# Kernel tuning notes

Measured on AMD Instinct MI355X. Metric: run time of the kernel, lower is better.

## Reference

```python
import jax, jax.numpy as jnp
import numpy as np

S = 8192      # total packed tokens
H = 1152      # hidden size
NH = 16       # heads
HD = 72       # head dim
NSEG = 8      # number of packed (equal-length) sequences
L = S // NSEG # tokens per sequence
SCALE = HD ** -0.5


def setup_inputs() -> dict:
    key = jax.random.key(0)
    ks = jax.random.split(key, 4)
    hidden_states = jax.random.normal(ks[0], (1, S, H), jnp.float32)
    # Real rotary cos/sin per token position within each sequence.
    inv_freq = 1.0 / (10000.0 ** (np.arange(0, HD, 2, dtype=np.float64) / HD))
    freqs = np.outer(np.arange(L, dtype=np.float64), inv_freq)  # [L, HD/2]
    emb = np.concatenate([freqs, freqs], axis=-1)               # [L, HD]
    cos = jnp.asarray(np.tile(np.cos(emb), (NSEG, 1)), jnp.float32)  # [S, HD]
    sin = jnp.asarray(np.tile(np.sin(emb), (NSEG, 1)), jnp.float32)
    Wqkv = jax.random.normal(ks[1], (H, 3 * H), jnp.float32) * (H ** -0.5)
    bqkv = jnp.zeros((3 * H,), jnp.float32)
    Wout = jax.random.normal(ks[2], (H, H), jnp.float32) * (H ** -0.5)
    bout = jnp.zeros((H,), jnp.float32)
    cu_seqlens = jnp.arange(NSEG + 1, dtype=jnp.int32) * L
    return dict(hidden_states=hidden_states, cos=cos, sin=sin,
                Wqkv=Wqkv, bqkv=bqkv, Wout=Wout, bout=bout,
                cu_seqlens=cu_seqlens)


def _rotate_half(x):
    return jnp.concatenate([-x[..., HD // 2:], x[..., :HD // 2]], axis=-1)


def reference(hidden_states, cos, sin, Wqkv, bqkv, Wout, bout, cu_seqlens):
    # QKV projection (fused)
    qkv = hidden_states @ Wqkv + bqkv                 # [1, S, 3H]
    q, k, v = jnp.split(qkv, [H, 2 * H], axis=-1)
    q = q.reshape(1, S, NH, HD)
    k = k.reshape(1, S, NH, HD)
    v = v.reshape(1, S, NH, HD)
    # Inline RoPE on q/k (cos/sin broadcast over heads)
    c = cos[None, :, None, :]
    s = sin[None, :, None, :]
    q = q * c + _rotate_half(q) * s
    k = k * c + _rotate_half(k) * s
    # Varlen (block-diagonal) non-causal attention: equal-length segments
    q = q.reshape(NSEG, L, NH, HD)
    k = k.reshape(NSEG, L, NH, HD)
    v = v.reshape(NSEG, L, NH, HD)
    scores = jnp.einsum('nqhd,nkhd->nhqk', q, k) * SCALE  # [NSEG, NH, L, L]
    probs = jax.nn.softmax(scores, axis=-1)
    ctx = jnp.einsum('nhqk,nkhd->nqhd', probs, v)         # [NSEG, L, NH, HD]
    ctx = ctx.reshape(1, S, H)
    # Output projection
    return ctx @ Wout + bout
```

## Files before the change

### kernel.cpp

```cpp
#include <hip/hip_runtime.h>
#include <hip/hip_fp16.h>
#include <cstdint>

typedef _Float16 half8 __attribute__((ext_vector_type(8)));
typedef _Float16 half4 __attribute__((ext_vector_type(4)));
typedef float floatx4 __attribute__((ext_vector_type(4)));

#define S_TOT 8192
#define H_DIM 1152
#define NHEAD 16
#define HD 72
#define QSTR 96
#define KSTR 104
#define PSTR 76
#define VSTR 76
#define VT_TILE 6080
#define NSEG 8
#define SEGL 1024
#define QSCALE 0.17002324631230988f

__device__ __forceinline__ void gld_lds16(const void* g, void* l) {
  __builtin_amdgcn_global_load_lds((const __attribute__((address_space(1))) void*)g,
                                   (__attribute__((address_space(3))) void*)l, 16, 0, 0);
}

__global__ void cast_f32_f16(const float* __restrict__ in, _Float16* __restrict__ out, int n) {
  int i = (blockIdx.x * 256 + threadIdx.x) * 4;
  if (i < n) {
    float4 v = *(const float4*)(in + i);
    half4 o = { (_Float16)v.x, (_Float16)v.y, (_Float16)v.z, (_Float16)v.w };
    *(half4*)(out + i) = o;
  }
}

__global__ void transpose_cast(const float* __restrict__ W, _Float16* __restrict__ Wt,
                               int R, int C) {
  __shared__ float tile[32][33];
  int tx = threadIdx.x, ty = threadIdx.y;
  int bx = blockIdx.x, by = blockIdx.y;
#pragma unroll
  for (int i = 0; i < 4; ++i)
    tile[ty + i * 8][tx] = W[(size_t)(by * 32 + ty + i * 8) * C + bx * 32 + tx];
  __syncthreads();
#pragma unroll
  for (int i = 0; i < 4; ++i)
    Wt[(size_t)(bx * 32 + ty + i * 8) * R + by * 32 + tx] = (_Float16)tile[tx][ty + i * 8];
}

template <bool OUT_HALF>
__global__ __launch_bounds__(512, 2) void gemm256(
    const _Float16* __restrict__ A, const _Float16* __restrict__ Bt,
    const float* __restrict__ bias, float* __restrict__ Cf, _Float16* __restrict__ Ch,
    int M, int N, int K, int NT) {
  extern __shared__ half8 smem8[];
  char* smem = (char*)smem8;
  const int tid = threadIdx.x;
  const int lane = tid & 63;
  const int w = tid >> 6;
  const int quad = lane >> 4, l16 = lane & 15;
  const int wm = w >> 2, wn = w & 3;

  const int orig = blockIdx.x;
  const int xcd = orig & 7, widx = orig >> 3;
  const int mt = xcd * 4 + (widx & 3), nt = widx >> 2;
  const int m0 = mt * 256, n0 = nt * 256;

  const _Float16* pA[2];
  const _Float16* pB[2];
#pragma unroll
  for (int i = 0; i < 2; ++i) {
    int c = i * 512 + tid;
    int r = c >> 2, cs = c & 3;
    int col = ((cs ^ ((r >> 1) & 3)) << 3);
    pA[i] = A + (size_t)(m0 + r) * K + col;
    int br = n0 + r; if (br >= N) br = N - 1;
    pB[i] = Bt + (size_t)br * K + col;
  }
  const int st0 = tid * 16, st1 = tid * 16 + 8192;
  const int rsl = ((quad ^ ((l16 >> 1) & 3)) << 4);
  const int aoff = (wm * 128 + l16) * 64 + rsl;
  const int boff = 16384 + (wn * 64 + l16) * 64 + rsl;

  half8 afA[8], bfA[4], afB[8], bfB[4];
  floatx4 acc[8][4] = {};

#define STG_A(ds, kcol) { \
  gld_lds16(pA[0] + (kcol), smem + (ds) * 32768 + st0); \
  gld_lds16(pA[1] + (kcol), smem + (ds) * 32768 + st1); }
#define STG_B(ds, kcol) { \
  gld_lds16(pB[0] + (kcol), smem + (ds) * 32768 + 16384 + st0); \
  gld_lds16(pB[1] + (kcol), smem + (ds) * 32768 + 16384 + st1); }
#define LDB4(s, bfx) { \
  _Pragma("unroll") for (int in = 0; in < 4; ++in) \
    bfx[in] = *(const half8*)(smem + (s) * 32768 + boff + in * 1024); }
#define LDA8(s, afx) { \
  _Pragma("unroll") for (int j = 0; j < 8; ++j) \
    afx[j] = *(const half8*)(smem + (s) * 32768 + aoff + j * 1024); }
#define MFMA32(afx, bfx) { \
  __builtin_amdgcn_s_setprio(1); \
  _Pragma("unroll") for (int j = 0; j < 8; ++j) \
  _Pragma("unroll") for (int in = 0; in < 4; ++in) \
    acc[j][in] = \
      __builtin_amdgcn_mfma_f32_16x16x32_f16(afx[j], bfx[in], acc[j][in], 0, 0, 0); \
  __builtin_amdgcn_s_setprio(0); }
#define BAR() __builtin_amdgcn_s_barrier()
#define SBAR() __builtin_amdgcn_sched_barrier(0)
#define LGKM0() { asm volatile("s_waitcnt lgkmcnt(0)" ::: "memory"); SBAR(); }
#define VMWAIT(t) { \
  if ((t) + 3 < KT)        { asm volatile("s_waitcnt vmcnt(4)" ::: "memory"); } \
  else if ((t) + 3 == KT)  { asm volatile("s_waitcnt vmcnt(0)" ::: "memory"); } }

  STG_A(0, 0);  STG_B(0, 0);
  STG_A(1, 32); STG_B(1, 32);
  STG_A(2, 64); STG_B(2, 64);
  asm volatile("s_waitcnt vmcnt(4)" ::: "memory");
  BAR();
  LDB4(0, bfA); LDA8(0, afA);
  LGKM0();

  const int KT = K >> 5;
#pragma unroll 1
  for (int u = 0; u < KT; u += 2) {
    {
      const int rs = (u + 1) & 3, ws = (u + 3) & 3;
      LDB4(rs, bfB); LDA8(rs, afB);
      if (u + 3 < KT) { STG_A(ws, (u + 3) * 32); STG_B(ws, (u + 3) * 32); }
      SBAR();
      MFMA32(afA, bfA);
      SBAR();
      LGKM0();
      VMWAIT(u);
      BAR();
    }
    {
      const int rs = (u + 2) & 3, ws = (u + 4) & 3;
      if (u + 2 < KT) { LDB4(rs, bfA); LDA8(rs, afA); }
      if (u + 4 < KT) { STG_A(ws, (u + 4) * 32); STG_B(ws, (u + 4) * 32); }
      SBAR();
      MFMA32(afB, bfB);
      SBAR();
      LGKM0();
      VMWAIT(u + 1);
      if (u + 2 < KT) BAR();
    }
  }
#undef STG_A
#undef STG_B
#undef LDB4
#undef LDA8
#undef MFMA32
#undef BAR
#undef SBAR
#undef LGKM0
#undef VMWAIT

#pragma unroll
  for (int im = 0; im < 8; ++im) {
    int m = m0 + wm * 128 + im * 16 + quad * 4;
#pragma unroll
    for (int in = 0; in < 4; ++in) {
      int n = n0 + wn * 64 + in * 16 + l16;
      if (n < N) {
        float b = bias[n];
#pragma unroll
        for (int r = 0; r < 4; ++r) {
          float v = acc[im][in][r] + b;
          if (OUT_HALF) Ch[(size_t)(m + r) * N + n] = (_Float16)v;
          else          Cf[(size_t)(m + r) * N + n] = v;
        }
      }
    }
  }
}

template <bool OUT_HALF>
__global__ __launch_bounds__(256) void gemm_bt(
    const _Float16* __restrict__ A, const _Float16* __restrict__ Bt,
    const float* __restrict__ bias, float* __restrict__ Cf, _Float16* __restrict__ Ch,
    int M, int N, int K, int NT) {
  __shared__ __align__(16) _Float16 As[128 * 72];
  __shared__ __align__(16) _Float16 Bs[128 * 72];
  const int tid = threadIdx.x;
  const int lane = tid & 63, w = tid >> 6;
  const int quad = lane >> 4, l16 = lane & 15;
  const int wm = w >> 1, wn = w & 1;
  const int id = blockIdx.x;
  const int j = id & 7, k = id >> 3;
  const int nt_ = k % NT, mt_ = (k / NT) * 8 + j;
  const int m0 = mt_ * 128, n0 = nt_ * 128;

  int rowi[5], cci[5];
#pragma unroll
  for (int i = 0; i < 5; ++i) {
    int c = tid + i * 256;
    int r = c / 9, cc = c - r * 9;
    rowi[i] = r;
    cci[i] = (cc == 8) ? 0 : cc;
  }

  floatx4 acc[4][4] = {};

  for (int kt = 0; kt < K; kt += 64) {
    __syncthreads();
#pragma unroll
    for (int i = 0; i < 4; ++i) {
      gld_lds16(A + (size_t)(m0 + rowi[i]) * K + kt + cci[i] * 8, (char*)As + (tid + i * 256) * 16);
      gld_lds16(Bt + (size_t)(n0 + rowi[i]) * K + kt + cci[i] * 8, (char*)Bs + (tid + i * 256) * 16);
    }
    if (tid < 128) {
      gld_lds16(A + (size_t)(m0 + rowi[4]) * K + kt + cci[4] * 8, (char*)As + (tid + 1024) * 16);
      gld_lds16(Bt + (size_t)(n0 + rowi[4]) * K + kt + cci[4] * 8, (char*)Bs + (tid + 1024) * 16);
    }
    __syncthreads();
#pragma unroll
    for (int kk = 0; kk < 2; ++kk) {
      half8 af[4], bf[4];
#pragma unroll
      for (int im = 0; im < 4; ++im)
        af[im] = *(const half8*)&As[(wm * 64 + im * 16 + l16) * 72 + kk * 32 + quad * 8];
#pragma unroll
      for (int in = 0; in < 4; ++in)
        bf[in] = *(const half8*)&Bs[(wn * 64 + in * 16 + l16) * 72 + kk * 32 + quad * 8];
#pragma unroll
      for (int im = 0; im < 4; ++im)
#pragma unroll
        for (int in = 0; in < 4; ++in)
          acc[im][in] = __builtin_amdgcn_mfma_f32_16x16x32_f16(af[im], bf[in], acc[im][in], 0, 0, 0);
    }
  }
#pragma unroll
  for (int im = 0; im < 4; ++im) {
    int m = m0 + wm * 64 + im * 16 + quad * 4;
#pragma unroll
    for (int in = 0; in < 4; ++in) {
      int n = n0 + wn * 64 + in * 16 + l16;
      float b = bias[n];
#pragma unroll
      for (int r = 0; r < 4; ++r) {
        float v = acc[im][in][r] + b;
        if (OUT_HALF) Ch[(size_t)(m + r) * N + n] = (_Float16)v;
        else          Cf[(size_t)(m + r) * N + n] = v;
      }
    }
  }
}

__global__ __launch_bounds__(256) void rope_scatter(
    const _Float16* __restrict__ QKV,
    const float* __restrict__ cosb,
    const float* __restrict__ sinb,
    _Float16* __restrict__ Qo, _Float16* __restrict__ Ko) {
  __shared__ __align__(16) _Float16 Ls[256 * 120];
  const int tid = threadIdx.x;
  const int t0 = blockIdx.x * 256;
  const int t = t0 + tid;
  const int l = t & 1023, h = (t >> 10) & 15, n = t >> 14;
  const int s = n * SEGL + l;
  const _Float16* q = QKV + (size_t)s * 3456 + h * HD;
  const _Float16* k = q + H_DIM;
  const float* cs = cosb + (size_t)s * HD;
  const float* sn = sinb + (size_t)s * HD;
  half8 z = {};
  {
    _Float16 qr[72], qv[72];
#pragma unroll
    for (int i = 0; i < 9; ++i) *(half8*)&qr[8 * i] = *(const half8*)(q + 8 * i);
#pragma unroll
    for (int d = 0; d < 36; ++d) {
      float c0 = cs[d], s0 = sn[d], c1 = cs[d + 36], s1 = sn[d + 36];
      float a = (float)qr[d], b = (float)qr[d + 36];
      qv[d]      = (_Float16)((a * c0 - b * s0) * QSCALE);
      qv[d + 36] = (_Float16)((b * c1 + a * s1) * QSCALE);
    }
#pragma unroll
    for (int i = 0; i < 9; ++i) *(half8*)&Ls[tid * 104 + 8 * i] = *(half8*)&qv[8 * i];
#pragma unroll
    for (int i = 9; i < 12; ++i) *(half8*)&Ls[tid * 104 + 8 * i] = z;
  }
  __syncthreads();
  {
    _Float16* dst = Qo + (size_t)t0 * QSTR;
#pragma unroll
    for (int it = 0; it < 12; ++it) {
      int j = tid + it * 256;
      int row = j / 12, c = j - row * 12;
      *(half8*)(dst + (size_t)j * 8) = *(const half8*)&Ls[row * 104 + c * 8];
    }
  }
  __syncthreads();
  {
    _Float16 kr[72], kv[72];
#pragma unroll
    for (int i = 0; i < 9; ++i) *(half8*)&kr[8 * i] = *(const half8*)(k + 8 * i);
#pragma unroll
    for (int d = 0; d < 36; ++d) {
      float c0 = cs[d], s0 = sn[d], c1 = cs[d + 36], s1 = sn[d + 36];
      float a = (float)kr[d], b = (float)kr[d + 36];
      kv[d]      = (_Float16)(a * c0 - b * s0);
      kv[d + 36] = (_Float16)(b * c1 + a * s1);
    }
#pragma unroll
    for (int i = 0; i < 9; ++i) *(half8*)&Ls[tid * 120 + 8 * i] = *(half8*)&kv[8 * i];
#pragma unroll
    for (int i = 9; i < 13; ++i) *(half8*)&Ls[tid * 120 + 8 * i] = z;
  }
  __syncthreads();
  {
    _Float16* dst = Ko + (size_t)t0 * KSTR;
#pragma unroll
    for (int it = 0; it < 13; ++it) {
      int j = tid + it * 256;
      int row = j / 13, c = j - row * 13;
      *(half8*)(dst + (size_t)j * 8) = *(const half8*)&Ls[row * 120 + c * 8];
    }
  }
}

__global__ __launch_bounds__(256) void transpose_v(const _Float16* __restrict__ QKV,
                                                   _Float16* __restrict__ Vt) {
  __shared__ __align__(16) _Float16 Vs[64 * 88];
  const int tid = threadIdx.x;
  const int kb = blockIdx.x, h = blockIdx.y, n = blockIdx.z;
  const int s0 = n * SEGL + kb * 64;
  const _Float16* src = QKV + (size_t)s0 * 3456 + 2 * H_DIM + h * HD;
  for (int idx = tid; idx < 576; idx += 256) {
    int key = idx / 9, c = idx - key * 9;
    *(half8*)&Vs[key * 88 + c * 8] = *(const half8*)(src + (size_t)key * 3456 + c * 8);
  }
  __syncthreads();
  _Float16* dst = Vt + (((size_t)(n * NHEAD + h)) * 16 + kb) * VT_TILE;
  for (int idx = tid; idx < 800; idx += 256) {
    int d = idx / 10, c = idx - d * 10;
    if (c < 8) {
      half8 v = {};
      if (d < HD) {
#pragma unroll
        for (int j = 0; j < 8; ++j) v[j] = Vs[(c * 8 + j) * 88 + d];
      } else if (d == HD) {
#pragma unroll
        for (int j = 0; j < 8; ++j) v[j] = (_Float16)1.0f;
      }
      *(half8*)(dst + d * VSTR + c * 8) = v;
    } else if (c == 8) {
      *(half8*)(dst + d * VSTR + 64) = half8{};
    } else {
      *(half4*)(dst + d * VSTR + 72) = half4{};
    }
  }
}

__global__ __launch_bounds__(256, 3) void attn_kernel(
    const _Float16* __restrict__ Qb, const _Float16* __restrict__ Kb,
    const _Float16* __restrict__ Vtb, _Float16* __restrict__ Ctx) {
  __shared__ __align__(16) _Float16 Kt[64 * KSTR];
  __shared__ __align__(16) _Float16 Vt[80 * VSTR];
  __shared__ __align__(16) _Float16 Ps[4 * 16 * PSTR];
  const int tid = threadIdx.x;
  const int lane = tid & 63, w = tid >> 6;
  const int quad = lane >> 4, l16 = lane & 15;
  const int id = blockIdx.x;
  const int hn = id & 127, qb = id >> 7;
  const int h = hn >> 3, n = hn & 7;
  const size_t hseg = (size_t)(n * NHEAD + h);
  const _Float16* Qg = Qb + hseg * SEGL * QSTR;
  const _Float16* Kg = Kb + hseg * SEGL * KSTR;
  const _Float16* Vg = Vtb + hseg * 16 * VT_TILE;

  half8 qf[2][3];
#pragma unroll
  for (int qg = 0; qg < 2; ++qg) {
    int row = qb * 128 + w * 32 + qg * 16 + l16;
#pragma unroll
    for (int kc = 0; kc < 3; ++kc)
      qf[qg][kc] = *(const half8*)(Qg + (size_t)row * QSTR + kc * 32 + quad * 8);
  }
  floatx4 o_acc[2][5] = {};

  for (int kb = 0; kb < SEGL / 64; ++kb) {
    __syncthreads();
    {
      const char* base = (const char*)(Kg + (size_t)kb * 64 * KSTR);
#pragma unroll
      for (int i = 0; i < 3; ++i)
        gld_lds16(base + tid * 16 + i * 4096, (char*)Kt + tid * 16 + i * 4096);
      if (tid < 64)
        gld_lds16(base + 12288 + tid * 16, (char*)Kt + 12288 + tid * 16);
    }
    {
      const char* base = (const char*)(Vg + (size_t)kb * VT_TILE);
#pragma unroll
      for (int i = 0; i < 2; ++i)
        gld_lds16(base + tid * 16 + i * 4096, (char*)Vt + tid * 16 + i * 4096);
      if (tid < 248)
        gld_lds16(base + 8192 + tid * 16, (char*)Vt + 8192 + tid * 16);
    }
    __syncthreads();
    floatx4 sa[2][4] = {};
    __builtin_amdgcn_s_setprio(1);
#pragma unroll
    for (int nt = 0; nt < 4; ++nt) {
      half8 kf[3];
#pragma unroll
      for (int kc = 0; kc < 3; ++kc)
        kf[kc] = *(const half8*)&Kt[(nt * 16 + l16) * KSTR + kc * 32 + quad * 8];
#pragma unroll
      for (int qg = 0; qg < 2; ++qg)
#pragma unroll
        for (int kc = 0; kc < 3; ++kc)
          sa[qg][nt] = __builtin_amdgcn_mfma_f32_16x16x32_f16(kf[kc], qf[qg][kc], sa[qg][nt], 0, 0, 0);
    }
    __builtin_amdgcn_s_setprio(0);
#pragma unroll
    for (int qg = 0; qg < 2; ++qg)
#pragma unroll
      for (int nt = 0; nt < 4; ++nt)
#pragma unroll
        for (int r = 0; r < 4; ++r)
          sa[qg][nt][r] = exp2f(sa[qg][nt][r]);
    half8 vf[2][5];
#pragma unroll
    for (int kc2 = 0; kc2 < 2; ++kc2)
#pragma unroll
      for (int t = 0; t < 5; ++t)
        vf[kc2][t] = *(const half8*)&Vt[(t * 16 + l16) * VSTR + kc2 * 32 + quad * 8];
#pragma unroll
    for (int qg = 0; qg < 2; ++qg) {
      int prow = (w * 16 + l16) * PSTR;
#pragma unroll
      for (int nt = 0; nt < 4; ++nt) {
        half4 ph = { (_Float16)sa[qg][nt][0], (_Float16)sa[qg][nt][1],
                     (_Float16)sa[qg][nt][2], (_Float16)sa[qg][nt][3] };
        *(half4*)&Ps[prow + nt * 16 + quad * 4] = ph;
      }
      __builtin_amdgcn_s_setprio(1);
#pragma unroll
      for (int kc2 = 0; kc2 < 2; ++kc2) {
        half8 pb = *(const half8*)&Ps[(w * 16 + l16) * PSTR + kc2 * 32 + quad * 8];
#pragma unroll
        for (int t = 0; t < 5; ++t)
          o_acc[qg][t] = __builtin_amdgcn_mfma_f32_16x16x32_f16(vf[kc2][t], pb, o_acc[qg][t], 0, 0, 0);
      }
      __builtin_amdgcn_s_setprio(0);
    }
  }
#pragma unroll
  for (int qg = 0; qg < 2; ++qg) {
    float lsum = __shfl(o_acc[qg][4][0], 32 + l16, 64);
    float rl = 1.0f / lsum;
    size_t s2 = (size_t)n * SEGL + qb * 128 + w * 32 + qg * 16 + l16;
#pragma unroll
    for (int t = 0; t < 5; ++t) {
      int d0 = t * 16 + quad * 4;
      if (d0 < HD) {
        half4 hv = { (_Float16)(o_acc[qg][t][0] * rl), (_Float16)(o_acc[qg][t][1] * rl),
                     (_Float16)(o_acc[qg][t][2] * rl), (_Float16)(o_acc[qg][t][3] * rl) };
        *(half4*)&Ctx[s2 * H_DIM + h * HD + d0] = hv;
      }
    }
  }
}

extern "C" void kernel_launch(void* const* d_in, const int* in_sizes, int n_in,
                              void* d_out, int out_size, void* d_ws, size_t ws_size,
                              hipStream_t stream) {
  const float* X    = (const float*)d_in[0];
  const float* cosb = (const float*)d_in[1];
  const float* sinb = (const float*)d_in[2];
  const float* Wqkv = (const float*)d_in[3];
  const float* bqkv = (const float*)d_in[4];
  const float* Wout = (const float*)d_in[5];
  const float* bout = (const float*)d_in[6];
  float* out = (float*)d_out;
  char* ws = (char*)d_ws;

  _Float16* Xb   = (_Float16*)(ws);
  _Float16* Wqt  = (_Float16*)(ws + 18874368);
  _Float16* Wot  = (_Float16*)(ws + 26836992);
  _Float16* QKVb = (_Float16*)(ws + 29491200);
  _Float16* Qb   = (_Float16*)(ws + 86114304);
  _Float16* Kb   = (_Float16*)(ws + 111280128);
  _Float16* Vtb  = (_Float16*)(ws + 138543104);
  _Float16* Ctx  = Xb;

  static bool attr_done = false;
  if (!attr_done) {
    hipFuncSetAttribute(reinterpret_cast<const void*>(gemm256<true>),
                        hipFuncAttributeMaxDynamicSharedMemorySize, 131072);
    attr_done = true;
  }

  cast_f32_f16<<<9216, 256, 0, stream>>>(X, Xb, S_TOT * H_DIM);
  transpose_cast<<<dim3(108, 36), dim3(32, 8), 0, stream>>>(Wqkv, Wqt, H_DIM, 3 * H_DIM);
  transpose_cast<<<dim3(36, 36), dim3(32, 8), 0, stream>>>(Wout, Wot, H_DIM, H_DIM);
  gemm256<true><<<448, 512, 131072, stream>>>(Xb, Wqt, bqkv, nullptr, QKVb,
                                              S_TOT, 3 * H_DIM, H_DIM, 14);
  rope_scatter<<<512, 256, 0, stream>>>(QKVb, cosb, sinb, Qb, Kb);
  transpose_v<<<dim3(16, 16, 8), 256, 0, stream>>>(QKVb, Vtb);
  attn_kernel<<<1024, 256, 0, stream>>>(Qb, Kb, Vtb, Ctx);
  gemm_bt<false><<<576, 256, 0, stream>>>(Ctx, Wot, bout, out, nullptr,
                                          S_TOT, H_DIM, H_DIM, 9);
}
```

Baseline: 354.1 us.

## Fuse V transpose into rope kernel and double-buffer K tiles in attention

The V-transpose kernel is merged into rope_scatter: each block of 256 tokens of one head also writes the four matching 64-key V^T tiles, staged through the shared buffer it already has, which saves one kernel launch. In the attention kernel, K tiles are now double-buffered so the next tile's load is issued before the current QK^T compute. The barrier after the loads moves to after the exp step, so the V load can overlap the score math. Doubling the K buffer in LDS may lower occupancy, and the moved barrier relies on the async LDS loads having completed by that point.

```diff
diff --git a/kernel.cpp b/kernel.cpp
--- a/kernel.cpp
+++ b/kernel.cpp
@@ -249,12 +249,14 @@
     const _Float16* __restrict__ QKV,
     const float* __restrict__ cosb,
     const float* __restrict__ sinb,
-    _Float16* __restrict__ Qo, _Float16* __restrict__ Ko) {
+    _Float16* __restrict__ Qo, _Float16* __restrict__ Ko,
+    _Float16* __restrict__ Vt) {
   __shared__ __align__(16) _Float16 Ls[256 * 120];
   const int tid = threadIdx.x;
   const int t0 = blockIdx.x * 256;
   const int t = t0 + tid;
   const int l = t & 1023, h = (t >> 10) & 15, n = t >> 14;
+  const int l0 = t0 & 1023;
   const int s = n * SEGL + l;
   const _Float16* q = QKV + (size_t)s * 3456 + h * HD;
   const _Float16* k = q + H_DIM;
@@ -314,37 +316,36 @@
       *(half8*)(dst + (size_t)j * 8) = *(const half8*)&Ls[row * 120 + c * 8];
     }
   }
-}
-
-__global__ __launch_bounds__(256) void transpose_v(const _Float16* __restrict__ QKV,
-                                                   _Float16* __restrict__ Vt) {
-  __shared__ __align__(16) _Float16 Vs[64 * 88];
-  const int tid = threadIdx.x;
-  const int kb = blockIdx.x, h = blockIdx.y, n = blockIdx.z;
-  const int s0 = n * SEGL + kb * 64;
-  const _Float16* src = QKV + (size_t)s0 * 3456 + 2 * H_DIM + h * HD;
-  for (int idx = tid; idx < 576; idx += 256) {
-    int key = idx / 9, c = idx - key * 9;
-    *(half8*)&Vs[key * 88 + c * 8] = *(const half8*)(src + (size_t)key * 3456 + c * 8);
-  }
   __syncthreads();
-  _Float16* dst = Vt + (((size_t)(n * NHEAD + h)) * 16 + kb) * VT_TILE;
-  for (int idx = tid; idx < 800; idx += 256) {
-    int d = idx / 10, c = idx - d * 10;
-    if (c < 8) {
-      half8 v = {};
-      if (d < HD) {
-#pragma unroll
-        for (int j = 0; j < 8; ++j) v[j] = Vs[(c * 8 + j) * 88 + d];
-      } else if (d == HD) {
-#pragma unroll
-        for (int j = 0; j < 8; ++j) v[j] = (_Float16)1.0f;
+  {
+    const _Float16* vsrc = QKV + (size_t)(n * SEGL + l0) * 3456 + 2 * H_DIM + h * HD;
+    for (int idx = tid; idx < 2304; idx += 256) {
+      int key = idx / 9, c = idx - key * 9;
+      *(half8*)&Ls[key * 88 + c * 8] = *(const half8*)(vsrc + (size_t)key * 3456 + c * 8);
+    }
+  }
+  __syncthreads();
+  {
+    _Float16* dst0 = Vt + (((size_t)(n * NHEAD + h)) * 16 + (l0 >> 6)) * VT_TILE;
+    for (int idx = tid; idx < 3200; idx += 256) {
+      int sub = idx / 800, rem = idx - sub * 800;
+      int d = rem / 10, c = rem - d * 10;
+      _Float16* dst = dst0 + sub * VT_TILE;
+      if (c < 8) {
+        half8 v = {};
+        if (d < HD) {
+#pragma unroll
+          for (int j = 0; j < 8; ++j) v[j] = Ls[(sub * 64 + c * 8 + j) * 88 + d];
+        } else if (d == HD) {
+#pragma unroll
+          for (int j = 0; j < 8; ++j) v[j] = (_Float16)1.0f;
+        }
+        *(half8*)(dst + d * VSTR + c * 8) = v;
+      } else if (c == 8) {
+        *(half8*)(dst + d * VSTR + 64) = half8{};
+      } else {
+        *(half4*)(dst + d * VSTR + 72) = half4{};
       }
-      *(half8*)(dst + d * VSTR + c * 8) = v;
-    } else if (c == 8) {
-      *(half8*)(dst + d * VSTR + 64) = half8{};
-    } else {
-      *(half4*)(dst + d * VSTR + 72) = half4{};
     }
   }
 }
@@ -352,7 +353,7 @@
 __global__ __launch_bounds__(256, 3) void attn_kernel(
     const _Float16* __restrict__ Qb, const _Float16* __restrict__ Kb,
     const _Float16* __restrict__ Vtb, _Float16* __restrict__ Ctx) {
-  __shared__ __align__(16) _Float16 Kt[64 * KSTR];
+  __shared__ __align__(16) _Float16 Kt[2][64 * KSTR];
   __shared__ __align__(16) _Float16 Vt[80 * VSTR];
   __shared__ __align__(16) _Float16 Ps[4 * 16 * PSTR];
   const int tid = threadIdx.x;
@@ -376,15 +377,25 @@
   }
   floatx4 o_acc[2][5] = {};
 
+  {
+    const char* base = (const char*)Kg;
+#pragma unroll
+    for (int i = 0; i < 3; ++i)
+      gld_lds16(base + tid * 16 + i * 4096, (char*)Kt[0] + tid * 16 + i * 4096);
+    if (tid < 64)
+      gld_lds16(base + 12288 + tid * 16, (char*)Kt[0] + 12288 + tid * 16);
+  }
+
   for (int kb = 0; kb < SEGL / 64; ++kb) {
     __syncthreads();
-    {
-      const char* base = (const char*)(Kg + (size_t)kb * 64 * KSTR);
+    if (kb + 1 < SEGL / 64) {
+      const char* base = (const char*)(Kg + (size_t)(kb + 1) * 64 * KSTR);
+      char* dst = (char*)Kt[(kb + 1) & 1];
 #pragma unroll
       for (int i = 0; i < 3; ++i)
-        gld_lds16(base + tid * 16 + i * 4096, (char*)Kt + tid * 16 + i * 4096);
+        gld_lds16(base + tid * 16 + i * 4096, dst + tid * 16 + i * 4096);
       if (tid < 64)
-        gld_lds16(base + 12288 + tid * 16, (char*)Kt + 12288 + tid * 16);
+        gld_lds16(base + 12288 + tid * 16, dst + 12288 + tid * 16);
     }
     {
       const char* base = (const char*)(Vg + (size_t)kb * VT_TILE);
@@ -394,7 +405,7 @@
       if (tid < 248)
         gld_lds16(base + 8192 + tid * 16, (char*)Vt + 8192 + tid * 16);
     }
-    __syncthreads();
+    const _Float16* Kc = Kt[kb & 1];
     floatx4 sa[2][4] = {};
     __builtin_amdgcn_s_setprio(1);
 #pragma unroll
@@ -402,7 +413,7 @@
       half8 kf[3];
 #pragma unroll
       for (int kc = 0; kc < 3; ++kc)
-        kf[kc] = *(const half8*)&Kt[(nt * 16 + l16) * KSTR + kc * 32 + quad * 8];
+        kf[kc] = *(const half8*)&Kc[(nt * 16 + l16) * KSTR + kc * 32 + quad * 8];
 #pragma unroll
       for (int qg = 0; qg < 2; ++qg)
 #pragma unroll
@@ -417,6 +428,7 @@
 #pragma unroll
         for (int r = 0; r < 4; ++r)
           sa[qg][nt][r] = exp2f(sa[qg][nt][r]);
+    __syncthreads();
     half8 vf[2][5];
 #pragma unroll
     for (int kc2 = 0; kc2 < 2; ++kc2)
@@ -494,8 +506,7 @@
   transpose_cast<<<dim3(36, 36), dim3(32, 8), 0, stream>>>(Wout, Wot, H_DIM, H_DIM);
   gemm256<true><<<448, 512, 131072, stream>>>(Xb, Wqt, bqkv, nullptr, QKVb,
                                               S_TOT, 3 * H_DIM, H_DIM, 14);
-  rope_scatter<<<512, 256, 0, stream>>>(QKVb, cosb, sinb, Qb, Kb);
-  transpose_v<<<dim3(16, 16, 8), 256, 0, stream>>>(QKVb, Vtb);
+  rope_scatter<<<512, 256, 0, stream>>>(QKVb, cosb, sinb, Qb, Kb, Vtb);
   attn_kernel<<<1024, 256, 0, stream>>>(Qb, Kb, Vtb, Ctx);
   gemm_bt<false><<<576, 256, 0, stream>>>(Ctx, Wot, bout, out, nullptr,
                                           S_TOT, H_DIM, H_DIM, 9);
```

Result: no change. 356.5 us (+0.7%).
